# Kernel tuning notes

Measured on AMD Instinct MI355X. Metric: run time of the kernel, lower is better.

Reference implementation:

```python
import jax, jax.numpy as jnp
import numpy as np

WINDOW = 256  # attention_window (band half-width w; band is 2w+1 wide)


def _longformer(q, k, v, global_attention_mask, padding_mask, num_global, w):
    B, H, S, D = q.shape
    BH = B * H
    G = int(num_global)
    scale = jnp.sqrt(jnp.asarray(D, q.dtype))
    qf = q.reshape(BH, S, D)
    kf = k.reshape(BH, S, D)
    vf = v.reshape(BH, S, D)
    is_global = jnp.repeat(global_attention_mask.astype(bool), H, axis=0)  # [BH,S]
    pad_ok = jnp.repeat(padding_mask.astype(bool), H, axis=0)              # [BH,S]
    NEG = jnp.asarray(-jnp.inf, q.dtype)

    # ---- banded local qk scores via overlapping 3-chunk trick ----
    nc = S // w
    qc = qf.reshape(BH, nc, w, D)
    kp = jnp.pad(kf, ((0, 0), (w, w), (0, 0))).reshape(BH, nc + 2, w, D)
    k3 = jnp.concatenate([kp[:, :-2], kp[:, 1:-1], kp[:, 2:]], axis=2)     # [BH,nc,3w,D]
    scores3 = jnp.einsum('bcxd,bcyd->bcxy', qc, k3) / scale                # [BH,nc,w,3w]
    band_idx = jnp.arange(w)[:, None] + jnp.arange(2 * w + 1)[None, :]     # [w,2w+1]
    band = jnp.take_along_axis(scores3, band_idx[None, None], axis=3)
    band = band.reshape(BH, S, 2 * w + 1)                                  # score[i,t] = q_i . k_{i-w+t}

    # ---- local-band masking: out-of-bounds, global key columns, padding ----
    rel = jnp.arange(S)[:, None] + jnp.arange(-w, w + 1)[None, :]          # [S,2w+1]
    oob = (rel < 0) | (rel >= S)
    relc = jnp.clip(rel, 0, S - 1)
    glob_key = is_global[:, relc]                                          # [BH,S,2w+1]
    pad_key = pad_ok[:, relc]
    band = jnp.where(oob[None] | glob_key | ~pad_key, NEG, band)

    # ---- all tokens attend to the (sparse) global keys ----
    gpos = jnp.argsort((~is_global).astype(jnp.int32), axis=-1)[:, :G]     # stable: global positions in order
    gk = jnp.take_along_axis(kf, gpos[..., None], axis=1)                  # [BH,G,D]
    gv = jnp.take_along_axis(vf, gpos[..., None], axis=1)
    g_ok = jnp.take_along_axis(pad_ok, gpos, axis=1)                       # [BH,G]
    gscores = jnp.einsum('bsd,bgd->bsg', qf, gk) / scale
    gscores = jnp.where(g_ok[:, None, :], gscores, NEG)

    # ---- joint softmax over [global | local band] ----
    probs = jax.nn.softmax(jnp.concatenate([gscores, band], axis=-1), axis=-1)
    gprobs, lprobs = probs[..., :G], probs[..., G:]

    ctx = jnp.einsum('bsg,bgd->bsd', gprobs, gv)
    vp = jnp.pad(vf, ((0, 0), (w, w), (0, 0))).reshape(BH, nc + 2, w, D)
    v3 = jnp.concatenate([vp[:, :-2], vp[:, 1:-1], vp[:, 2:]], axis=2)     # [BH,nc,3w,D]
    p3 = jnp.zeros((BH, nc, w, 3 * w), probs.dtype)
    p3 = p3.at[:, :, jnp.arange(w)[:, None], band_idx].set(lprobs.reshape(BH, nc, w, 2 * w + 1))
    ctx = ctx + jnp.einsum('bcxy,bcyd->bcxd', p3, v3).reshape(BH, S, D)

    # ---- global tokens attend to every token (full attention rows) ----
    gq = jnp.take_along_axis(qf, gpos[..., None], axis=1)                  # [BH,G,D]
    rscores = jnp.einsum('bgd,bsd->bgs', gq, kf) / scale
    rscores = jnp.where(pad_ok[:, None, :], rscores, NEG)
    rprobs = jax.nn.softmax(rscores, axis=-1)
    vmask = jnp.where(pad_ok[..., None], vf, jnp.asarray(0.0, vf.dtype))
    ctx_g = jnp.einsum('bgs,bsd->bgd', rprobs, vmask)
    ctx = ctx.at[jnp.arange(BH)[:, None], gpos].set(ctx_g)

    return ctx.reshape(B, H, S, D)


def setup_inputs() -> dict:
    key = jax.random.key(0)
    kq, kk, kv = jax.random.split(key, 3)
    B, H, S, D, G = 1, 16, 4096, 64, 64
    q = jax.random.normal(kq, (B, H, S, D), jnp.float32)
    k = jax.random.normal(kk, (B, H, S, D), jnp.float32)
    v = jax.random.normal(kv, (B, H, S, D), jnp.float32)
    global_attention_mask = jnp.zeros((B, S), jnp.int32).at[:, :G].set(1)
    padding_mask = jnp.ones((B, S), jnp.int32)
    return {"q": q, "k": k, "v": v, "global_attention_mask": global_attention_mask,
            "padding_mask": padding_mask, "num_global": G}


def reference(q, k, v, global_attention_mask, padding_mask, num_global):
    return _longformer(q, k, v, global_attention_mask, padding_mask, num_global, WINDOW)
```

## Files before the change

### kernel.cpp

```cpp
#include <hip/hip_runtime.h>
#include <hip/hip_bf16.h>

#define SLEN 4096
#define NH   16
#define DH   64
#define WW   256
#define GMAX 64

typedef unsigned short u16;
typedef unsigned int   u32;
typedef unsigned long long u64;
typedef __attribute__((ext_vector_type(8))) short bf16x8;
typedef __attribute__((ext_vector_type(4))) float f32x4;

#define MFMA16(a,b,c) __builtin_amdgcn_mfma_f32_16x16x32_bf16((a),(b),(c),0,0,0)

static __device__ __forceinline__ int imin(int a, int b) { return a < b ? a : b; }
static __device__ __forceinline__ int imax(int a, int b) { return a > b ? a : b; }

__device__ __forceinline__ u32 cvtpk(float lo, float hi) {
  u32 r;
  asm("v_cvt_pk_bf16_f32 %0, %1, %2" : "=v"(r) : "v"(lo), "v"(hi));
  return r;
}
__device__ __forceinline__ u16 f2bf(float x) {
  u32 u = __float_as_uint(x);
  u32 r = (u + 0x7fffu + ((u >> 16) & 1u)) >> 16;
  return (u16)r;
}

__device__ __forceinline__ void gload16(const u16* src, u16* lds_base) {
  __builtin_amdgcn_global_load_lds((const __attribute__((address_space(1))) u32*)src,
                                   (__attribute__((address_space(3))) u32*)lds_base,
                                   16, 0, 0);
}

__global__ __launch_bounds__(256) void lf_prep1(
    const float* __restrict__ k, const float* __restrict__ v,
    const int* __restrict__ gmask, const int* __restrict__ pmask, const int* __restrict__ nGp,
    u16* __restrict__ kB, u16* __restrict__ vtB,
    int* __restrict__ gpos, unsigned char* __restrict__ gmsk,
    unsigned char* __restrict__ msk, unsigned char* __restrict__ cleanmap) {
  const int bid = blockIdx.x;
  const int tid = threadIdx.x;
  if (bid < 2048) {
    int i = (bid * 256 + tid) * 8;
    float4 v0 = *(const float4*)(k + i);
    float4 v1 = *(const float4*)(k + i + 4);
    uint4 w;
    w.x = cvtpk(v0.x, v0.y);
    w.y = cvtpk(v0.z, v0.w);
    w.z = cvtpk(v1.x, v1.y);
    w.w = cvtpk(v1.z, v1.w);
    *(uint4*)(kB + i) = w;
    return;
  }
  if (bid < 3072) {
    __shared__ float t[64][65];
    int b = bid - 2048;
    int h = b >> 6, s0 = (b & 63) << 6;
    int tile = h * 64 + (b & 63);
    int r = tid >> 2, c0 = (tid & 3) << 4;
    const float* src = v + ((size_t)h * SLEN + s0 + r) * DH + c0;
#pragma unroll
    for (int j = 0; j < 16; j += 4) {
      float4 a = *(const float4*)(src + j);
      t[r][c0 + j]     = a.x;
      t[r][c0 + j + 1] = a.y;
      t[r][c0 + j + 2] = a.z;
      t[r][c0 + j + 3] = a.w;
    }
    __syncthreads();
    int d = tid >> 2, j0 = (tid & 3) << 4;
    int grp  = j0 & 32;
    int half = (j0 & 16) ? 4 : 0;
    u16* dst = vtB + ((size_t)tile * 64 + d) * 64 + grp;
#pragma unroll
    for (int q4 = 0; q4 < 4; ++q4) {
      uint2 val;
      val.x = cvtpk(t[j0 + 4 * q4 + 0][d], t[j0 + 4 * q4 + 1][d]);
      val.y = cvtpk(t[j0 + 4 * q4 + 2][d], t[j0 + 4 * q4 + 3][d]);
      *(uint2*)(dst + 8 * q4 + half) = val;
    }
    return;
  }
  const int G = imin(nGp[0], GMAX);
  for (int s = tid; s < SLEN; s += 256) {
    unsigned char b = (unsigned char)((pmask[s] ? 1 : 0) | (gmask[s] ? 2 : 0));
    msk[s] = b;
  }
  for (int s = SLEN + tid; s < SLEN + 64; s += 256) msk[s] = 0;
  __syncthreads();
  if (tid < 64) {
    int lane = tid;
    if (lane < GMAX) gmsk[lane] = 0;
    int cnt = 0;
    for (int c = 0; c < SLEN / 64 && cnt < G; ++c) {
      int s = c * 64 + lane;
      bool isg = gmask[s] != 0;
      u64 b = __ballot(isg);
      int rank = cnt + (int)__popcll(b & ((1ull << lane) - 1ull));
      if (isg && rank < G) gpos[rank] = s;
      cnt += (int)__popcll(b);
    }
    if (cnt < G) {
      int fill = cnt;
      for (int c = 0; c < SLEN / 64 && fill < G; ++c) {
        int s = c * 64 + lane;
        bool non = gmask[s] == 0;
        u64 b = __ballot(non);
        int rank = fill + (int)__popcll(b & ((1ull << lane) - 1ull));
        if (non && rank < G) gpos[rank] = s;
        fill += (int)__popcll(b);
      }
    }
  }
  __syncthreads();
  if (tid < 64) {
    if (tid < G) {
      int p = gpos[tid];
      gmsk[tid] = (unsigned char)(pmask[p] ? 1 : 0);
      msk[p] = (unsigned char)(msk[p] | 4);
    }
  } else if (tid >= 128) {
    int c = tid - 128;
    if (c < SLEN / 32) {
      unsigned char ok1 = 1, ok2 = 1;
      for (int kk = 0; kk < 32; ++kk) {
        unsigned char b = msk[c * 32 + kk];
        ok1 &= (unsigned char)(((b & 3) == 1) ? 1 : 0);
        ok2 &= (unsigned char)(b & 1);
      }
      cleanmap[c] = (unsigned char)(ok1 | (ok2 << 1));
    }
  }
}

__global__ void lf_gather(const float* __restrict__ qF, const u16* __restrict__ kB,
                          const u16* __restrict__ vtB, const int* __restrict__ gpos,
                          const int* __restrict__ nGp,
                          u16* __restrict__ gq, u16* __restrict__ gk, u16* __restrict__ gvt,
                          float qscale) {
  const int G = imin(nGp[0], GMAX);
  int idx = blockIdx.x * 256 + threadIdx.x;
  int h = idx >> 12, m = (idx >> 6) & 63, d = idx & 63;
  size_t oq = ((size_t)h * GMAX + m) * DH + d;
  int r = m & 31;
  int pos = ((r & 12) << 1) + ((r & 16) >> 2) + (r & 3);
  size_t ot = ((size_t)h * DH + d) * GMAX + (m & 32) + pos;
  if (m < G) {
    int p = gpos[m];
    int pr = p & 31;
    int ppos = ((pr & 12) << 1) + ((pr & 16) >> 2) + (pr & 3);
    gq[oq]  = f2bf(qF[((size_t)h * SLEN + p) * DH + d] * qscale);
    gk[oq]  = kB[((size_t)h * SLEN + p) * DH + d];
    gvt[ot] = vtB[((size_t)(h * 64 + (p >> 6)) * 64 + d) * 64 + (p & 32) + ppos];
  } else {
    gq[oq] = 0; gk[oq] = 0; gvt[ot] = 0;
  }
}

__global__ __launch_bounds__(256) void lf_attn(
    const float* __restrict__ qF, const u16* __restrict__ kB, const u16* __restrict__ vtB,
    const u16* __restrict__ gkB, const u16* __restrict__ gqB, const u16* __restrict__ gvtB,
    const unsigned char* __restrict__ gmskA, const unsigned char* __restrict__ mskA,
    const unsigned char* __restrict__ cleanA, const int* __restrict__ nGp,
    float* __restrict__ out, float* __restrict__ pAcc, float* __restrict__ pL, float qscale) {
  __shared__ __align__(16) u16 sK[3][4096];
  __shared__ __align__(16) u16 sV[3][4096];

  const int tid  = threadIdx.x;
  const int wv   = tid >> 6;
  const int lane = tid & 63;
  const int ql   = lane & 15;
  const int g    = lane >> 4;
  const float NEGV = -1e30f;
  const float MEXP = 24.0f;
  const int G = imin(nGp[0], GMAX);

  const int wg = ((int)blockIdx.x & 7) * 144 + ((int)blockIdx.x >> 3);
  const bool glob = (wg % 9) == 0;

  int off[4][2];
#pragma unroll
  for (int t = 0; t < 4; ++t)
#pragma unroll
    for (int c = 0; c < 2; ++c) {
      int row = 16 * t + ql;
      off[t][c] = (row * 8 + ((c * 4 + g) ^ (row & 7))) * 8;
    }

  f32x4 acc[4];
#pragma unroll
  for (int i = 0; i < 4; ++i) acc[i] = (f32x4){0.f, 0.f, 0.f, 0.f};
  f32x4 lsv = (f32x4){0.f, 0.f, 0.f, 0.f};
  bf16x8 qf0, qf1;

  int h, s0w = 0, sq = 0, t0, nPh, qg = 0, splitIdx = 0;
  int lo_w = 0, hi_w = 0;
  bool hasG = false;
  const u16 *gks = nullptr, *gvs = nullptr;

  if (!glob) {
    int lid = wg - wg / 9 - 1;
    h = lid >> 6;
    int qblk = lid & 63;
    int s0 = qblk << 6;
    s0w = s0 + 16 * wv; sq = s0w + ql;
    t0 = imax(0, qblk - 4);
    int t1 = imin(63, qblk + 4);
    nPh = t1 - t0 + 1;
    hasG = (G > 0);
    lo_w = imax(t0, (s0w - WW) >> 6);
    hi_w = imin(t1, (s0w + 15 + WW) >> 6);
    const float* qr = qF + ((size_t)h * SLEN + sq) * DH;
    float4 a0 = *(const float4*)(qr + 8 * g);
    float4 a1 = *(const float4*)(qr + 8 * g + 4);
    float4 b0 = *(const float4*)(qr + 32 + 8 * g);
    float4 b1 = *(const float4*)(qr + 32 + 8 * g + 4);
    union { u32 w[4]; bf16x8 v; } uq;
    uq.w[0] = cvtpk(a0.x * qscale, a0.y * qscale);
    uq.w[1] = cvtpk(a0.z * qscale, a0.w * qscale);
    uq.w[2] = cvtpk(a1.x * qscale, a1.y * qscale);
    uq.w[3] = cvtpk(a1.z * qscale, a1.w * qscale);
    qf0 = uq.v;
    uq.w[0] = cvtpk(b0.x * qscale, b0.y * qscale);
    uq.w[1] = cvtpk(b0.z * qscale, b0.w * qscale);
    uq.w[2] = cvtpk(b1.x * qscale, b1.y * qscale);
    uq.w[3] = cvtpk(b1.z * qscale, b1.w * qscale);
    qf1 = uq.v;
    gks = gkB + (size_t)h * GMAX * DH;
    gvs = gvtB + (size_t)h * 4096;
  } else {
    int gb = wg / 9;
    h = gb >> 3; splitIdx = gb & 7;
    qg = wv * 16 + ql;
    t0 = splitIdx * 8; nPh = 8;
    const u16* qRow = gqB + ((size_t)h * GMAX + qg) * DH;
    qf0 = *(const bf16x8*)(qRow + 8 * g);
    qf1 = *(const bf16x8*)(qRow + 32 + 8 * g);
  }
  const u16* kbase = kB  + (size_t)h * 64 * 4096;
  const u16* vbase = vtB + (size_t)h * 64 * 4096;
  const int totPh = nPh + (hasG ? 1 : 0);

  auto stage = [&](int p, int b) {
    const u16 *ks, *vs;
    if (hasG && p == 0) { ks = gks; vs = gvs; }
    else {
      int tv = t0 + p - (hasG ? 1 : 0);
      ks = kbase + (size_t)tv * 4096;
      vs = vbase + (size_t)tv * 4096;
    }
#pragma unroll
    for (int j = 0; j < 2; ++j) {
      int gran = (wv * 2 + j) * 64 + lane;
      int sg = gran ^ ((gran >> 3) & 7);
      gload16(ks + (size_t)sg * 8, &sK[b][(wv * 2 + j) * 512]);
      gload16(vs + (size_t)sg * 8, &sV[b][(wv * 2 + j) * 512]);
    }
  };

  auto compute = [&](int p, int buf) {
    const bool isg = (hasG && p == 0);
    const int tv = t0 + p - (hasG ? 1 : 0);
    const int kb = tv * 64;
    bool doC = glob ? true : (isg || (tv >= lo_w && tv <= hi_w));
    if (!doC) return;
    const u16* sk = &sK[buf][0];
    const u16* sv = &sV[buf][0];
    f32x4 sc[4];
#pragma unroll
    for (int t = 0; t < 4; ++t) sc[t] = (f32x4){0.f, 0.f, 0.f, 0.f};
#pragma unroll
    for (int t = 0; t < 4; ++t) {
      bf16x8 a0 = *(const bf16x8*)(sk + off[t][0]);
      bf16x8 a1 = *(const bf16x8*)(sk + off[t][1]);
      sc[t] = MFMA16(a0, qf0, sc[t]);
      sc[t] = MFMA16(a1, qf1, sc[t]);
    }
    f32x4 pv[4];
    if (isg) {
#pragma unroll
      for (int t = 0; t < 4; ++t) {
        u32 mw = *(const u32*)(gmskA + 16 * t + 4 * g);
#pragma unroll
        for (int i = 0; i < 4; ++i) {
          float s = ((mw >> (8 * i)) & 1) ? sc[t][i] : NEGV;
          pv[t][i] = __builtin_amdgcn_exp2f(s - MEXP);
        }
      }
    } else if (glob) {
      u16 cw = *(const u16*)(cleanA + (kb >> 5));
      if (cw & (cw >> 8) & 2) {
#pragma unroll
        for (int t = 0; t < 4; ++t)
#pragma unroll
          for (int i = 0; i < 4; ++i)
            pv[t][i] = __builtin_amdgcn_exp2f(sc[t][i] - MEXP);
      } else {
#pragma unroll
        for (int t = 0; t < 4; ++t) {
          u32 mw = *(const u32*)(mskA + kb + 16 * t + 4 * g);
#pragma unroll
          for (int i = 0; i < 4; ++i) {
            float s = ((mw >> (8 * i)) & 1) ? sc[t][i] : NEGV;
            pv[t][i] = __builtin_amdgcn_exp2f(s - MEXP);
          }
        }
      }
    } else {
      u16 cw = *(const u16*)(cleanA + (kb >> 5));
      bool cl = ((cw & (cw >> 8) & 1) != 0) &&
                (kb >= s0w + 15 - WW) && (kb + 63 <= s0w + WW);
      if (cl) {
#pragma unroll
        for (int t = 0; t < 4; ++t)
#pragma unroll
          for (int i = 0; i < 4; ++i)
            pv[t][i] = __builtin_amdgcn_exp2f(sc[t][i] - MEXP);
      } else {
#pragma unroll
        for (int t = 0; t < 4; ++t) {
          u32 mw = *(const u32*)(mskA + kb + 16 * t + 4 * g);
#pragma unroll
          for (int i = 0; i < 4; ++i) {
            int kkey = kb + 16 * t + 4 * g + i;
            bool vok = (((mw >> (8 * i)) & 3) == 1) && (kkey >= sq - WW) && (kkey <= sq + WW);
            float s = vok ? sc[t][i] : NEGV;
            pv[t][i] = __builtin_amdgcn_exp2f(s - MEXP);
          }
        }
      }
    }
    lsv += pv[0] + pv[1] + pv[2] + pv[3];
#pragma unroll
    for (int s2 = 0; s2 < 2; ++s2) {
      union { u32 w[4]; bf16x8 v8; } u;
      u.w[0] = cvtpk(pv[2 * s2][0], pv[2 * s2][1]);
      u.w[1] = cvtpk(pv[2 * s2][2], pv[2 * s2][3]);
      u.w[2] = cvtpk(pv[2 * s2 + 1][0], pv[2 * s2 + 1][1]);
      u.w[3] = cvtpk(pv[2 * s2 + 1][2], pv[2 * s2 + 1][3]);
#pragma unroll
      for (int dt = 0; dt < 4; ++dt) {
        bf16x8 vf = *(const bf16x8*)(sv + off[dt][s2]);
        acc[dt] = MFMA16(vf, u.v8, acc[dt]);
      }
    }
  };

  stage(0, 0);
  if (totPh > 1) stage(1, 1);
  int cur = 0;
  for (int p = 0; p < totPh; ++p) {
    if (p + 1 < totPh) {
      asm volatile("s_waitcnt vmcnt(4)" ::: "memory");
    } else {
      asm volatile("s_waitcnt vmcnt(0)" ::: "memory");
    }
    __builtin_amdgcn_s_barrier();
    __builtin_amdgcn_sched_barrier(0);
    if (p + 2 < totPh) {
      int nb = cur + 2; if (nb >= 3) nb -= 3;
      stage(p + 2, nb);
    }
    compute(p, cur);
    ++cur; if (cur == 3) cur = 0;
  }

  float lsum = lsv[0] + lsv[1] + lsv[2] + lsv[3];
  lsum += __shfl_xor(lsum, 16);
  lsum += __shfl_xor(lsum, 32);

  if (!glob) {
    float inv = 1.f / lsum;
    bool skip = (mskA[sq] & 4) != 0;
    if (!skip) {
      float* orow = out + ((size_t)h * SLEN + sq) * DH;
#pragma unroll
      for (int dt = 0; dt < 4; ++dt) {
        f32x4 o = acc[dt] * inv;
        *(f32x4*)(orow + dt * 16 + 4 * g) = o;
      }
    }
  } else {
    float* pa = pAcc + ((size_t)(h * 8 + splitIdx) * 64 + qg) * 64;
#pragma unroll
    for (int dt = 0; dt < 4; ++dt)
      *(f32x4*)&pa[dt * 16 + 4 * g] = acc[dt];
    if (g == 0) pL[(h * 8 + splitIdx) * 64 + qg] = lsum;
  }
}

__global__ void lf_gmerge(const float* __restrict__ pAcc, const float* __restrict__ pL,
                          const int* __restrict__ gpos, const int* __restrict__ nGp,
                          float* __restrict__ out) {
  const int G = imin(nGp[0], GMAX);
  int h = blockIdx.x;
  int tid = threadIdx.x;
#pragma unroll
  for (int it = 0; it < 4; ++it) {
    int v = tid + it * 256;
    int q = v >> 4, d4 = (v & 15) << 2;
    if (q >= G) continue;
    float L = 0.f;
    f32x4 a = (f32x4){0.f, 0.f, 0.f, 0.f};
#pragma unroll
    for (int s = 0; s < 8; ++s) {
      L += pL[(h * 8 + s) * 64 + q];
      a += *(const f32x4*)&pAcc[((size_t)(h * 8 + s) * 64 + q) * 64 + d4];
    }
    *(f32x4*)&out[((size_t)h * SLEN + gpos[q]) * DH + d4] = a * (1.f / L);
  }
}

extern "C" void kernel_launch(void* const* d_in, const int* in_sizes, int n_in,
                              void* d_out, int out_size, void* d_ws, size_t ws_size,
                              hipStream_t stream) {
  const float* q = (const float*)d_in[0];
  const float* k = (const float*)d_in[1];
  const float* v = (const float*)d_in[2];
  const int* gmask = (const int*)d_in[3];
  const int* pmask = (const int*)d_in[4];
  const int* nGp = (const int*)d_in[5];
  float* out = (float*)d_out;
  char* ws = (char*)d_ws;

  constexpr size_t NEL = (size_t)NH * SLEN * DH;
  constexpr size_t OFF_KBF  = 0;
  constexpr size_t OFF_VTBF = OFF_KBF + NEL * 2;
  constexpr size_t OFF_GK   = OFF_VTBF + NEL * 2 + 256;
  constexpr size_t OFF_GQ   = OFF_GK + (size_t)NH * GMAX * DH * 2;
  constexpr size_t OFF_GVT  = OFF_GQ + (size_t)NH * GMAX * DH * 2;
  constexpr size_t OFF_GPOS = OFF_GVT + (size_t)NH * DH * GMAX * 2;
  constexpr size_t OFF_GMSK = OFF_GPOS + 256;
  constexpr size_t OFF_MSK  = OFF_GMSK + 64;
  constexpr size_t OFF_CLEAN = OFF_MSK + SLEN + 64;
  constexpr size_t OFF_PACC = OFF_CLEAN + 256;
  constexpr size_t OFF_PL   = OFF_PACC + (size_t)NH * 8 * 64 * 64 * 4;

  u16* kB  = (u16*)(ws + OFF_KBF);
  u16* vtB = (u16*)(ws + OFF_VTBF);
  u16* gk  = (u16*)(ws + OFF_GK);
  u16* gq  = (u16*)(ws + OFF_GQ);
  u16* gvt = (u16*)(ws + OFF_GVT);
  int* gpos = (int*)(ws + OFF_GPOS);
  unsigned char* gmsk = (unsigned char*)(ws + OFF_GMSK);
  unsigned char* msk  = (unsigned char*)(ws + OFF_MSK);
  unsigned char* clean = (unsigned char*)(ws + OFF_CLEAN);
  float* pAcc = (float*)(ws + OFF_PACC);
  float* pL   = (float*)(ws + OFF_PL);

  const float qscale = 0.125f * 1.4426950408889634f;

  lf_prep1<<<3073, 256, 0, stream>>>(k, v, gmask, pmask, nGp,
                                     kB, vtB, gpos, gmsk, msk, clean);
  lf_gather<<<256, 256, 0, stream>>>(q, kB, vtB, gpos, nGp, gq, gk, gvt, qscale);
  lf_attn<<<1152, 256, 0, stream>>>(q, kB, vtB, gk, gq, gvt, gmsk, msk, clean,
                                    nGp, out, pAcc, pL, qscale);
  lf_gmerge<<<NH, 256, 0, stream>>>(pAcc, pL, gpos, nGp, out);
}
```

Before: 55.25 us.

## Switch to double-buffered K/V staging and preload masks into shared memory

The K/V staging ring shrinks from three LDS buffers to two. Each phase now issues the next tile's load before waiting and adds a second barrier after compute to protect buffer reuse. Per-tile mask words and global mask words are loaded once into shared memory, and the clean-tile flags are collapsed into one wavefront ballot bitmask, which removes per-phase global mask loads. The aims are lower LDS use, possibly higher occupancy, and fewer scattered global loads in the inner loop. The cost is a shallower prefetch depth and an extra barrier every phase.

```diff
diff --git a/kernel.cpp b/kernel.cpp
--- a/kernel.cpp
+++ b/kernel.cpp
@@ -166,8 +166,10 @@
     const unsigned char* __restrict__ gmskA, const unsigned char* __restrict__ mskA,
     const unsigned char* __restrict__ cleanA, const int* __restrict__ nGp,
     float* __restrict__ out, float* __restrict__ pAcc, float* __restrict__ pL, float qscale) {
-  __shared__ __align__(16) u16 sK[3][4096];
-  __shared__ __align__(16) u16 sV[3][4096];
+  __shared__ __align__(16) u16 sK[2][4096];
+  __shared__ __align__(16) u16 sV[2][4096];
+  __shared__ u32 sMsk[192];
+  __shared__ u32 sGm[16];
 
   const int tid  = threadIdx.x;
   const int wv   = tid >> 6;
@@ -196,7 +198,7 @@
   f32x4 lsv = (f32x4){0.f, 0.f, 0.f, 0.f};
   bf16x8 qf0, qf1;
 
-  int h, s0w = 0, sq = 0, t0, nPh, qg = 0, splitIdx = 0;
+  int h, s0w = 0, sq = 0, t0, nMain, qg = 0, splitIdx = 0;
   int lo_w = 0, hi_w = 0;
   bool hasG = false;
   const u16 *gks = nullptr, *gvs = nullptr;
@@ -209,7 +211,7 @@
     s0w = s0 + 16 * wv; sq = s0w + ql;
     t0 = imax(0, qblk - 4);
     int t1 = imin(63, qblk + 4);
-    nPh = t1 - t0 + 1;
+    nMain = t1 - t0 + 1;
     hasG = (G > 0);
     lo_w = imax(t0, (s0w - WW) >> 6);
     hi_w = imin(t1, (s0w + 15 + WW) >> 6);
@@ -235,14 +237,21 @@
     int gb = wg / 9;
     h = gb >> 3; splitIdx = gb & 7;
     qg = wv * 16 + ql;
-    t0 = splitIdx * 8; nPh = 8;
+    t0 = splitIdx * 8; nMain = 8;
     const u16* qRow = gqB + ((size_t)h * GMAX + qg) * DH;
     qf0 = *(const bf16x8*)(qRow + 8 * g);
     qf1 = *(const bf16x8*)(qRow + 32 + 8 * g);
   }
   const u16* kbase = kB  + (size_t)h * 64 * 4096;
   const u16* vbase = vtB + (size_t)h * 64 * 4096;
-  const int totPh = nPh + (hasG ? 1 : 0);
+  const int totPh = nMain + (hasG ? 1 : 0);
+
+  const unsigned char cmask = glob ? 2 : 1;
+  unsigned char cbyte = 0;
+  if (lane < nMain) {
+    cbyte = (unsigned char)(cleanA[2 * (t0 + lane)] & cleanA[2 * (t0 + lane) + 1]);
+  }
+  const u64 cbits = __ballot((cbyte & cmask) != 0);
 
   auto stage = [&](int p, int b) {
     const u16 *ks, *vs;
@@ -263,7 +272,8 @@
 
   auto compute = [&](int p, int buf) {
     const bool isg = (hasG && p == 0);
-    const int tv = t0 + p - (hasG ? 1 : 0);
+    const int idx = p - (hasG ? 1 : 0);
+    const int tv = t0 + idx;
     const int kb = tv * 64;
     bool doC = glob ? true : (isg || (tv >= lo_w && tv <= hi_w));
     if (!doC) return;
@@ -283,46 +293,36 @@
     if (isg) {
 #pragma unroll
       for (int t = 0; t < 4; ++t) {
-        u32 mw = *(const u32*)(gmskA + 16 * t + 4 * g);
+        u32 mw = sGm[4 * t + g];
 #pragma unroll
         for (int i = 0; i < 4; ++i) {
           float s = ((mw >> (8 * i)) & 1) ? sc[t][i] : NEGV;
           pv[t][i] = __builtin_amdgcn_exp2f(s - MEXP);
         }
       }
-    } else if (glob) {
-      u16 cw = *(const u16*)(cleanA + (kb >> 5));
-      if (cw & (cw >> 8) & 2) {
+    } else {
+      bool cl = ((cbits >> idx) & 1) != 0;
+      if (!glob) cl = cl && (kb >= s0w + 15 - WW) && (kb + 63 <= s0w + WW);
+      if (cl) {
 #pragma unroll
         for (int t = 0; t < 4; ++t)
 #pragma unroll
           for (int i = 0; i < 4; ++i)
             pv[t][i] = __builtin_amdgcn_exp2f(sc[t][i] - MEXP);
-      } else {
+      } else if (glob) {
 #pragma unroll
         for (int t = 0; t < 4; ++t) {
-          u32 mw = *(const u32*)(mskA + kb + 16 * t + 4 * g);
+          u32 mw = sMsk[(idx << 4) + 4 * t + g];
 #pragma unroll
           for (int i = 0; i < 4; ++i) {
             float s = ((mw >> (8 * i)) & 1) ? sc[t][i] : NEGV;
             pv[t][i] = __builtin_amdgcn_exp2f(s - MEXP);
           }
         }
-      }
-    } else {
-      u16 cw = *(const u16*)(cleanA + (kb >> 5));
-      bool cl = ((cw & (cw >> 8) & 1) != 0) &&
-                (kb >= s0w + 15 - WW) && (kb + 63 <= s0w + WW);
-      if (cl) {
-#pragma unroll
-        for (int t = 0; t < 4; ++t)
-#pragma unroll
-          for (int i = 0; i < 4; ++i)
-            pv[t][i] = __builtin_amdgcn_exp2f(sc[t][i] - MEXP);
       } else {
 #pragma unroll
         for (int t = 0; t < 4; ++t) {
-          u32 mw = *(const u32*)(mskA + kb + 16 * t + 4 * g);
+          u32 mw = sMsk[(idx << 4) + 4 * t + g];
 #pragma unroll
           for (int i = 0; i < 4; ++i) {
             int kkey = kb + 16 * t + 4 * g + i;
@@ -350,22 +350,24 @@
   };
 
   stage(0, 0);
-  if (totPh > 1) stage(1, 1);
-  int cur = 0;
+  {
+    int nb = nMain << 4;
+    if (tid < nb) sMsk[tid] = *(const u32*)(mskA + (t0 << 6) + (tid << 2));
+    if (hasG && tid >= 192 && tid < 208) sGm[tid - 192] = *(const u32*)(gmskA + ((tid - 192) << 2));
+  }
+  __syncthreads();
+
   for (int p = 0; p < totPh; ++p) {
     if (p + 1 < totPh) {
+      stage(p + 1, (p + 1) & 1);
       asm volatile("s_waitcnt vmcnt(4)" ::: "memory");
     } else {
       asm volatile("s_waitcnt vmcnt(0)" ::: "memory");
     }
     __builtin_amdgcn_s_barrier();
     __builtin_amdgcn_sched_barrier(0);
-    if (p + 2 < totPh) {
-      int nb = cur + 2; if (nb >= 3) nb -= 3;
-      stage(p + 2, nb);
-    }
-    compute(p, cur);
-    ++cur; if (cur == 3) cur = 0;
+    compute(p, p & 1);
+    __builtin_amdgcn_s_barrier();
   }
 
   float lsum = lsv[0] + lsv[1] + lsv[2] + lsv[3];
```

New measurement: 53.37 us. -3.4%, faster.
